# Performance work log

Hardware: AMD Instinct MI355X
Metric: run time of the kernel (lower is better)

Reference implementation:

```python
import jax, jax.numpy as jnp
import numpy as np

B, N, Hh, E = 16, 1024, 8, 64      # q/k/v: (B, N, H, E), H*E == ich
C, K, ICH, MODES = 64, 8, 512, 16  # c, k, ich, modes
IN_CH, OUT_CH, LVL = 64, 64, 0     # in_channels, out_channels, L


def fourier_cross_attn(q, k, v):
    """FourierCrossAttentionW with activation='tanh'. q,k,v: (B,L,E,H) -> (B,L,E,H).
    mode_select indices are range(min(L//2, modes)) -> contiguous low-mode slice.
    Note: v is unused in the original (only its length, equal to k's here)."""
    L = q.shape[1]
    xq = jnp.transpose(q, (0, 3, 2, 1))  # (B,H,E,L)
    xk = jnp.transpose(k, (0, 3, 2, 1))
    m = min(L // 2, MODES)
    xq_ft = jnp.fft.rfft(xq, axis=-1)[..., :m]   # (B,H,E,m) complex
    xk_ft = jnp.fft.rfft(xk, axis=-1)[..., :m]
    xqk = jnp.tanh(jnp.einsum('bhex,bhey->bhxy', xq_ft, xk_ft))  # complex tanh, (B,H,m,m)
    xqkv = jnp.einsum('bhxy,bhey->bhex', xqk, xk_ft)             # (B,H,E,m)
    pad = jnp.zeros(xqkv.shape[:-1] + (L // 2 + 1 - m,), xqkv.dtype)
    out_ft = jnp.concatenate([xqkv, pad], axis=-1)               # scatter low modes, rest zero
    out = jnp.fft.irfft(out_ft / (IN_CH * OUT_CH), n=L, axis=-1)
    return jnp.transpose(out, (0, 3, 2, 1))


def wavelet_transform(x, ec_d, ec_s):
    # x: (B, L, c, k) -> detail, approx each (B, L//2, c, k)
    xa = jnp.concatenate([x[:, ::2], x[:, 1::2]], axis=-1)  # (B, L/2, c, 2k)
    return xa @ ec_d, xa @ ec_s


def even_odd(x, rc_e, rc_o):
    # x: (B, L, c, 2k) -> (B, 2L, c, k), interleaving even/odd reconstructions
    b, n, c, _ = x.shape
    x_e = x @ rc_e  # (B,L,c,k)
    x_o = x @ rc_o
    return jnp.stack([x_e, x_o], axis=2).reshape(b, 2 * n, c, K)


def _forward(q, k, v, Lq_w, Lq_b, Lk_w, Lk_b, Lv_w, Lv_b, out_w, out_b,
             ec_s, ec_d, rc_e, rc_o):
    b, n, _, _ = q.shape
    s = k.shape[1]
    q = (q.reshape(b, n, ICH) @ Lq_w + Lq_b).reshape(b, n, C, K)
    k = (k.reshape(b, s, ICH) @ Lk_w + Lk_b).reshape(b, s, C, K)
    v = (v.reshape(b, s, ICH) @ Lv_w + Lv_b).reshape(b, s, C, K)
    if n > s:
        z = jnp.zeros((b, n - s, C, K), q.dtype)
        v = jnp.concatenate([v, z], axis=1)
        k = jnp.concatenate([k, z], axis=1)
    else:
        v = v[:, :n]
        k = k[:, :n]
    ns = int(np.floor(np.log2(n)))
    nl = 2 ** int(np.ceil(np.log2(n)))
    if nl > n:  # pad to power of two by wrapping leading entries
        q = jnp.concatenate([q, q[:, :nl - n]], axis=1)
        k = jnp.concatenate([k, k[:, :nl - n]], axis=1)
        v = jnp.concatenate([v, v[:, :nl - n]], axis=1)
    Ud, Us = [], []
    for _ in range(ns - LVL):
        dq, q = wavelet_transform(q, ec_d, ec_s)
        dk, k = wavelet_transform(k, ec_d, ec_s)
        dv, v = wavelet_transform(v, ec_d, ec_s)
        # original: attn1(d_q,d_k,d_v) + attn2(s_q,s_k,s_v); Us uses details (Us_q stores d)
        Ud.append(fourier_cross_attn(dq, dk, dv) + fourier_cross_attn(q, k, v))
        Us.append(fourier_cross_attn(dq, dk, dv))
    v = fourier_cross_attn(q, k, v)
    for i in range(ns - 1 - LVL, -1, -1):
        v = v + Us[i]
        v = jnp.concatenate([v, Ud[i]], axis=-1)
        v = even_odd(v, rc_e, rc_o)
    return v[:, :n].reshape(b, n, C * K) @ out_w + out_b


def setup_inputs() -> dict:
    key = jax.random.key(0)
    ks = jax.random.split(key, 16)
    f = jax.random.normal
    ws = 1.0 / np.sqrt(ICH)       # Linear init scale
    fs = 1.0 / np.sqrt(2 * K)     # wavelet filter scale (stand-in for legendre filters)
    return {
        'q': f(ks[0], (B, N, Hh, E), jnp.float32),
        'k': f(ks[1], (B, N, Hh, E), jnp.float32),
        'v': f(ks[2], (B, N, Hh, E), jnp.float32),
        'Lq_w': f(ks[3], (ICH, C * K), jnp.float32) * ws,
        'Lq_b': f(ks[4], (C * K,), jnp.float32) * ws,
        'Lk_w': f(ks[5], (ICH, C * K), jnp.float32) * ws,
        'Lk_b': f(ks[6], (C * K,), jnp.float32) * ws,
        'Lv_w': f(ks[7], (ICH, C * K), jnp.float32) * ws,
        'Lv_b': f(ks[8], (C * K,), jnp.float32) * ws,
        'out_w': f(ks[9], (C * K, ICH), jnp.float32) * ws,
        'out_b': f(ks[10], (ICH,), jnp.float32) * ws,
        'ec_s': f(ks[11], (2 * K, K), jnp.float32) * fs,
        'ec_d': f(ks[12], (2 * K, K), jnp.float32) * fs,
        'rc_e': f(ks[13], (2 * K, K), jnp.float32) * fs,
        'rc_o': f(ks[14], (2 * K, K), jnp.float32) * fs,
    }


def reference(q, k, v, Lq_w, Lq_b, Lk_w, Lk_b, Lv_w, Lv_b, out_w, out_b,
              ec_s, ec_d, rc_e, rc_o):
    return _forward(q, k, v, Lq_w, Lq_b, Lk_w, Lk_b, Lv_w, Lv_b,
                    out_w, out_b, ec_s, ec_d, rc_e, rc_o)
```

## Files before the change

kernel.cpp:

```cpp
#include <hip/hip_runtime.h>
#include <cstddef>

#define PI2F 6.283185307179586f

typedef __bf16 bf16_t;
typedef __bf16 bf16x8 __attribute__((ext_vector_type(8)));
typedef float f32x4 __attribute__((ext_vector_type(4)));

#define QA_OFF   0u
#define KA_OFF   8388608u
#define CH_OFF   16777216u
#define MF_OFF   (CH_OFF + 33488896u)
#define MUS_OFF  (MF_OFF + 9437184u)
#define MUD_OFF  (MUS_OFF + 2359296u)
#define WF_OFF   (MUD_OFF + 2359296u)
#define WI_OFF   (WF_OFF + 32704u)
#define WT_OFF   (WI_OFF + 32704u)

__global__ __launch_bounds__(256)
void wprep_k(const float* __restrict__ Wq, const float* __restrict__ Wk,
             const float* __restrict__ Wo, bf16_t* __restrict__ WT)
{
    __shared__ float T[32][33];
    const int w = blockIdx.x >> 8;
    const int tile = blockIdx.x & 255;
    const int k0 = (tile & 15) * 32, n0 = (tile >> 4) * 32;
    const float* W = (w == 0) ? Wq : (w == 1) ? Wk : Wo;
    bf16_t* oh = WT + (size_t)w * 524288;
    bf16_t* ol = oh + 262144;
    const int tid = threadIdx.x;
    {
        int row = tid >> 3, q = tid & 7;
        float4 v = *(const float4*)(W + (size_t)(k0 + row) * 512 + n0 + q * 4);
        T[row][q*4+0] = v.x; T[row][q*4+1] = v.y; T[row][q*4+2] = v.z; T[row][q*4+3] = v.w;
    }
    __syncthreads();
    {
        int nr = tid >> 3, q = tid & 7;
        union { bf16_t b[4]; uint2 u; } ph, pl;
#pragma unroll
        for (int j = 0; j < 4; ++j) {
            float x = T[q*4+j][nr];
            bf16_t h = (bf16_t)x;
            ph.b[j] = h;
            pl.b[j] = (bf16_t)(x - (float)h);
        }
        size_t dst = (size_t)(n0 + nr) * 512 + k0 + q * 4;
        *(uint2*)&oh[dst] = ph.u;
        *(uint2*)&ol[dst] = pl.u;
    }
}

template<bool TOUT>
__global__ __launch_bounds__(256)
void mfma_gemm_k(const float* __restrict__ X, const bf16_t* __restrict__ WTh,
                 const bf16_t* __restrict__ WTl, const float* __restrict__ bias,
                 float* __restrict__ out)
{
    __shared__ __align__(16) char smem[40960];
    bf16_t* Ah = (bf16_t*)smem;
    bf16_t* Al = Ah + 128 * 40;
    bf16_t* Bh = Al + 128 * 40;
    bf16_t* Bl = Bh + 128 * 40;
    float* Cs = (float*)smem;
    const int tid = threadIdx.x;
    const int lane = tid & 63;
    const int wv = tid >> 6;
    const int wm = wv & 1, wn = wv >> 1;
    const int m0 = blockIdx.x << 7, n0 = blockIdx.y << 7;
    const int l15 = lane & 15, quad = lane >> 4;

    f32x4 acc[4][4];
    f32x4 zz = {0.f, 0.f, 0.f, 0.f};
#pragma unroll
    for (int i = 0; i < 4; ++i)
#pragma unroll
        for (int j = 0; j < 4; ++j) acc[i][j] = zz;

    for (int kc = 0; kc < 16; ++kc) {
#pragma unroll
        for (int i = 0; i < 4; ++i) {
            int u = tid + i * 256;
            int row = u >> 3, seg = u & 7;
            float4 v = *(const float4*)(X + (size_t)(m0 + row) * 512 + kc * 32 + seg * 4);
            union { bf16_t b[4]; uint2 u2; } ph, pl;
            float xs[4] = {v.x, v.y, v.z, v.w};
#pragma unroll
            for (int j = 0; j < 4; ++j) {
                bf16_t h = (bf16_t)xs[j];
                ph.b[j] = h;
                pl.b[j] = (bf16_t)(xs[j] - (float)h);
            }
            *(uint2*)&Ah[row * 40 + seg * 4] = ph.u2;
            *(uint2*)&Al[row * 40 + seg * 4] = pl.u2;
        }
#pragma unroll
        for (int i = 0; i < 4; ++i) {
            int u = tid + i * 256;
            int variant = u >> 9;
            int rs = u & 511;
            int row = rs >> 2, seg = rs & 3;
            const bf16_t* src = (variant ? WTl : WTh) + (size_t)(n0 + row) * 512 + kc * 32 + seg * 8;
            bf16_t* dst = (variant ? Bl : Bh) + row * 40 + seg * 8;
            *(float4*)dst = *(const float4*)src;
        }
        __syncthreads();
        bf16x8 ah[4], al[4];
#pragma unroll
        for (int mi = 0; mi < 4; ++mi) {
            int row = wm * 64 + mi * 16 + l15;
            ah[mi] = *(bf16x8*)&Ah[row * 40 + quad * 8];
            al[mi] = *(bf16x8*)&Al[row * 40 + quad * 8];
        }
#pragma unroll
        for (int ni = 0; ni < 4; ++ni) {
            int nr = wn * 64 + ni * 16 + l15;
            bf16x8 bh = *(bf16x8*)&Bh[nr * 40 + quad * 8];
            bf16x8 bl = *(bf16x8*)&Bl[nr * 40 + quad * 8];
#pragma unroll
            for (int mi = 0; mi < 4; ++mi) {
                acc[mi][ni] = __builtin_amdgcn_mfma_f32_16x16x32_bf16(ah[mi], bh, acc[mi][ni], 0, 0, 0);
                acc[mi][ni] = __builtin_amdgcn_mfma_f32_16x16x32_bf16(ah[mi], bl, acc[mi][ni], 0, 0, 0);
                acc[mi][ni] = __builtin_amdgcn_mfma_f32_16x16x32_bf16(al[mi], bh, acc[mi][ni], 0, 0, 0);
            }
        }
        __syncthreads();
    }

    if constexpr (TOUT) {
        const int b8 = (m0 >> 10) * 8, tb = m0 & 1023;
        for (int p = 0; p < 2; ++p) {
            if (wn == p) {
#pragma unroll
                for (int ni = 0; ni < 4; ++ni)
#pragma unroll
                    for (int mi = 0; mi < 4; ++mi)
#pragma unroll
                        for (int r = 0; r < 4; ++r) {
                            int nl = ni * 16 + l15;
                            int m = wm * 64 + mi * 16 + quad * 4 + r;
                            Cs[nl * 132 + m] = acc[mi][ni][r];
                        }
            }
            __syncthreads();
#pragma unroll
            for (int i = 0; i < 8; ++i) {
                int u = tid + i * 256;
                int col = u >> 5, seg = u & 31;
                int gc = n0 + p * 64 + col;
                float bz = bias[gc];
                float4 v = *(float4*)&Cs[col * 132 + seg * 4];
                v.x += bz; v.y += bz; v.z += bz; v.w += bz;
                int h = gc & 7, e = gc >> 3;
                *(float4*)(out + (((size_t)(b8 + h)) * 64 + e) * 1024 + tb + seg * 4) = v;
            }
            __syncthreads();
        }
    } else {
#pragma unroll
        for (int ni = 0; ni < 4; ++ni) {
            int n = n0 + wn * 64 + ni * 16 + l15;
            float bz = bias[n];
#pragma unroll
            for (int mi = 0; mi < 4; ++mi)
#pragma unroll
                for (int r = 0; r < 4; ++r) {
                    int m = m0 + wm * 64 + mi * 16 + quad * 4 + r;
                    out[(size_t)m * 512 + n] = acc[mi][ni][r] + bz;
                }
        }
    }
}

__global__ __launch_bounds__(256)
void twiddle_k(float* __restrict__ Wf, float* __restrict__ Wi)
{
    int idx = blockIdx.x * 256 + threadIdx.x;
    int table = idx / 32704;
    if (table >= 2) return;
    int r = idx - table * 32704;
    int lvl = 0, base = 0;
    for (int l = 0; l < 9; ++l) {
        int Ll = 512 >> l;
        int sz = 32 * Ll;
        if (r < base + sz) { lvl = l; break; }
        base += sz;
    }
    int L = 512 >> lvl;
    int rr = r - base;
    if (table == 0) {
        int t = rr >> 5, c = rr & 31;
        int j = c & 15, isIm = c >> 4;
        int mv = (j * t) & (L - 1);
        float ang = (PI2F / (float)L) * (float)mv;
        float s, cc; sincosf(ang, &s, &cc);
        Wf[r] = isIm ? -s : cc;
    } else {
        int k = rr / L, t = rr - (rr / L) * L;
        int j = k & 15, isIm = k >> 4;
        int mv = (j * t) & (L - 1);
        float ang = (PI2F / (float)L) * (float)mv;
        float s, cc; sincosf(ang, &s, &cc);
        float scale = 1.f / (4096.f * (float)L);
        float v;
        if (!isIm) v = (j == 0) ? 1.f : 2.f * cc;
        else       v = (j == 0) ? 0.f : -2.f * s;
        Wi[r] = v * scale;
    }
}

__global__ __launch_bounds__(256)
void wavelet_chain_k(const float* __restrict__ qin, const float* __restrict__ kin,
                     float* __restrict__ CH,
                     const float* __restrict__ ecd, const float* __restrict__ ecs)
{
    __shared__ float sA[8][520];
    __shared__ float sB[8][264];
    __shared__ float fd[128], fs[128];
    const int tid = threadIdx.x;
    const int tensor = blockIdx.x >> 10;
    const int b = (blockIdx.x >> 6) & 15;
    const int e = blockIdx.x & 63;
    const float* in = tensor ? kin : qin;
    if (tid < 128) fd[tid] = ecd[tid];
    else fs[tid - 128] = ecs[tid - 128];
    __syncthreads();

    const size_t rowd0 = (size_t)((tensor * 2 + 0) * 8192) + (size_t)(b * 8) * 64 + e;

    {
        const int L = 512;
#pragma unroll
        for (int it = 0; it < 2; ++it) {
            const int t = tid + it * 256;
            float xa[16];
#pragma unroll
            for (int h = 0; h < 8; ++h) {
                float2 v = *(const float2*)(in + ((size_t)((b*8 + h) * 64 + e)) * 1024 + 2 * t);
                xa[h] = v.x; xa[8 + h] = v.y;
            }
#pragma unroll
            for (int jj = 0; jj < 8; ++jj) {
                float ad = 0.f, as_ = 0.f;
#pragma unroll
                for (int rr = 0; rr < 16; ++rr) {
                    ad  = fmaf(xa[rr], fd[rr * 8 + jj], ad);
                    as_ = fmaf(xa[rr], fs[rr * 8 + jj], as_);
                }
                size_t rowd = rowd0 + (size_t)jj * 64;
                CH[rowd * L + t]          = ad;
                CH[(rowd + 8192) * L + t] = as_;
                sA[jj][t] = as_;
            }
        }
    }
    __syncthreads();

    float* cur = &sA[0][0]; int cs = 520;
    float* nxt = &sB[0][0]; int ns = 264;
    for (int lvl = 1; lvl < 9; ++lvl) {
        const int L = 512 >> lvl;
        const size_t chb = (size_t)32768 * (size_t)(1024 - 2 * L);
        if (tid < L) {
            const int t = tid;
            float xa[16];
#pragma unroll
            for (int h = 0; h < 8; ++h) {
                xa[h]     = cur[h * cs + 2 * t];
                xa[8 + h] = cur[h * cs + 2 * t + 1];
            }
#pragma unroll
            for (int jj = 0; jj < 8; ++jj) {
                float ad = 0.f, as_ = 0.f;
#pragma unroll
                for (int rr = 0; rr < 16; ++rr) {
                    ad  = fmaf(xa[rr], fd[rr * 8 + jj], ad);
                    as_ = fmaf(xa[rr], fs[rr * 8 + jj], as_);
                }
                size_t rowd = rowd0 + (size_t)jj * 64;
                CH[chb + rowd * L + t]          = ad;
                CH[chb + (rowd + 8192) * L + t] = as_;
                nxt[jj * ns + t] = as_;
            }
        }
        __syncthreads();
        float* tp = cur; cur = nxt; nxt = tp;
        int ts_ = cs; cs = ns; ns = ts_;
    }
}

__global__ __launch_bounds__(256)
void fwd_dft_k(const float* __restrict__ CH, const float* __restrict__ Wf,
               float* __restrict__ MF)
{
    __shared__ float As[32][132];
    __shared__ float Ws[32][36];
    const int tid = threadIdx.x;
    const int lvl = blockIdx.x >> 8;
    const int tile = blockIdx.x & 255;
    const int L = 512 >> lvl;
    const size_t chb = (size_t)32768 * (size_t)(1024 - 2 * L);
    const int wb = 32 * (1024 - 2 * L);
    const size_t mfb = (size_t)lvl * 1048576;
    const int rowb = tile * 128;
    const int rg = tid >> 3, cg = tid & 7;
    float acc[4][4] = {{0.f}};
    const int kw = (L < 32) ? L : 32;

    for (int k0 = 0; k0 < L; k0 += kw) {
        if (kw >= 4) {
            const int kq = kw >> 2;
            const int kqs = (kq == 8) ? 3 : (kq == 4) ? 2 : (kq == 2) ? 1 : 0;
            const int nf4 = 128 * kq;
            for (int u = tid; u < nf4; u += 256) {
                int row = u >> kqs, q = u & (kq - 1);
                float4 v = *(const float4*)(CH + chb + (size_t)(rowb + row) * L + k0 + q * 4);
                As[q*4+0][row] = v.x; As[q*4+1][row] = v.y;
                As[q*4+2][row] = v.z; As[q*4+3][row] = v.w;
            }
        } else {
            if (tid < 256) {
                int row = tid >> 1, t = tid & 1;
                As[t][row] = CH[chb + (size_t)(rowb + row) * 2 + t];
            }
        }
        for (int u = tid; u < kw * 8; u += 256) {
            int kr = u >> 3, q = u & 7;
            *(float4*)&Ws[kr][q * 4] = *(const float4*)&Wf[wb + (k0 + kr) * 32 + q * 4];
        }
        __syncthreads();
#pragma unroll 4
        for (int kk = 0; kk < kw; ++kk) {
            float4 a4 = *(float4*)&As[kk][rg * 4];
            float4 w4 = *(float4*)&Ws[kk][cg * 4];
            acc[0][0] = fmaf(a4.x, w4.x, acc[0][0]); acc[0][1] = fmaf(a4.x, w4.y, acc[0][1]);
            acc[0][2] = fmaf(a4.x, w4.z, acc[0][2]); acc[0][3] = fmaf(a4.x, w4.w, acc[0][3]);
            acc[1][0] = fmaf(a4.y, w4.x, acc[1][0]); acc[1][1] = fmaf(a4.y, w4.y, acc[1][1]);
            acc[1][2] = fmaf(a4.y, w4.z, acc[1][2]); acc[1][3] = fmaf(a4.y, w4.w, acc[1][3]);
            acc[2][0] = fmaf(a4.z, w4.x, acc[2][0]); acc[2][1] = fmaf(a4.z, w4.y, acc[2][1]);
            acc[2][2] = fmaf(a4.z, w4.z, acc[2][2]); acc[2][3] = fmaf(a4.z, w4.w, acc[2][3]);
            acc[3][0] = fmaf(a4.w, w4.x, acc[3][0]); acc[3][1] = fmaf(a4.w, w4.y, acc[3][1]);
            acc[3][2] = fmaf(a4.w, w4.z, acc[3][2]); acc[3][3] = fmaf(a4.w, w4.w, acc[3][3]);
        }
        __syncthreads();
    }
#pragma unroll
    for (int i = 0; i < 4; ++i) {
        float4 o = {acc[i][0], acc[i][1], acc[i][2], acc[i][3]};
        *(float4*)(MF + mfb + (size_t)(rowb + rg * 4 + i) * 32 + cg * 4) = o;
    }
}

__global__ __launch_bounds__(256)
void combine2_k(const float* __restrict__ MF, float* __restrict__ MUS, float* __restrict__ MUD)
{
    __shared__ float F[4][64][33];
    __shared__ float Sre[2][16][17], Sim[2][16][17];
    const int tid = threadIdx.x;
    const int lvl = blockIdx.x >> 7;
    const int bh = blockIdx.x & 127;
    const int L = 512 >> lvl;
    const int m = (L / 2 < 16) ? L / 2 : 16;
    const size_t mfb = (size_t)lvl * 1048576;
    for (int a = 0; a < 4; ++a) {
        const float* src = MF + mfb + ((size_t)a * 8192 + (size_t)bh * 64) * 32;
        for (int u = tid; u < 512; u += 256) {
            float4 v = *(const float4*)(src + u * 4);
            int ee = (u * 4) >> 5, c = (u * 4) & 31;
            F[a][ee][c] = v.x; F[a][ee][c+1] = v.y; F[a][ee][c+2] = v.z; F[a][ee][c+3] = v.w;
        }
    }
    __syncthreads();
    const int mm = m * m;
    for (int idx = tid; idx < 2 * mm; idx += 256) {
        int p = idx / mm, rr = idx - p * mm;
        int x = rr / m, y = rr - (rr / m) * m;
        float sr = 0.f, si = 0.f;
        for (int ee = 0; ee < 64; ++ee) {
            float qre = F[p][ee][x],     qim = F[p][ee][16 + x];
            float kre = F[2 + p][ee][y], kim = F[2 + p][ee][16 + y];
            sr = fmaf(qre, kre, sr); sr = fmaf(-qim, kim, sr);
            si = fmaf(qre, kim, si); si = fmaf(qim, kre, si);
        }
        float twoa = fminf(fmaxf(2.f * sr, -30.f), 30.f);
        float e2 = expf(twoa), inv = 1.f / e2;
        float s2b, c2b; sincosf(2.f * si, &s2b, &c2b);
        float den = 0.5f * (e2 + inv) + c2b;
        Sre[p][x][y] = 0.5f * (e2 - inv) / den;
        Sim[p][x][y] = s2b / den;
    }
    __syncthreads();
    for (int idx = tid; idx < 1024; idx += 256) {
        int ee = idx >> 4, x = idx & 15;
        float urd = 0.f, uid = 0.f, urs = 0.f, uis = 0.f;
        if (x < m) {
            for (int y = 0; y < m; ++y) {
                float k0re = F[2][ee][y], k0im = F[2][ee][16 + y];
                float k1re = F[3][ee][y], k1im = F[3][ee][16 + y];
                float s0r = Sre[0][x][y], s0i = Sim[0][x][y];
                float s1r = Sre[1][x][y], s1i = Sim[1][x][y];
                urd = fmaf(s0r, k0re, urd); urd = fmaf(-s0i, k0im, urd);
                uid = fmaf(s0r, k0im, uid); uid = fmaf(s0i, k0re, uid);
                urs = fmaf(s1r, k1re, urs); urs = fmaf(-s1i, k1im, urs);
                uis = fmaf(s1r, k1im, uis); uis = fmaf(s1i, k1re, uis);
            }
        }
        size_t mb = (size_t)lvl * 262144 + ((size_t)bh * 64 + ee) * 32;
        MUS[mb + x]      = urd;
        MUS[mb + 16 + x] = uid;
        MUD[mb + x]      = urd + urs;
        MUD[mb + 16 + x] = uid + uis;
    }
}

__global__ __launch_bounds__(256)
void inv_dft_k(const float* __restrict__ MUS, const float* __restrict__ MUD,
               const float* __restrict__ Wi,
               float* __restrict__ US, float* __restrict__ UD)
{
    __shared__ float As[32][132];
    __shared__ float Ws[32][36];
    const int bx = blockIdx.x;
    int lvl = 0, base = 0;
#pragma unroll
    for (int l = 0; l < 9; ++l) {
        int cl = 128 << ((l <= 4) ? (4 - l) : 0);
        if (bx < base + cl) { lvl = l; break; }
        base += cl;
    }
    const int r = bx - base;
    const int L = 512 >> lvl;
    const int tcb = (lvl <= 4) ? (4 - lvl) : 0;
    const int tile = r >> tcb;
    const int tc = r & ((1 << tcb) - 1);
    const int t0 = tc * 32;
    const int ar = tile >> 6;
    const int rowb = (tile & 63) * 128;
    const float* MU = ar ? MUD : MUS;
    float* OUT = ar ? UD : US;
    const int wb = 32 * (1024 - 2 * L);
    const size_t uoff = (size_t)8192 * (size_t)(1024 - 2 * L);
    const int nc = (L < 32) ? L : 32;
    const int tid = threadIdx.x;
    const int rg = tid >> 3, cg = tid & 7;

#pragma unroll
    for (int i = 0; i < 4; ++i) {
        int u = tid + i * 256;
        int row = u >> 3, q = u & 7;
        float4 v = *(const float4*)(MU + (size_t)lvl * 262144 + (size_t)(rowb + row) * 32 + q * 4);
        As[q*4+0][row] = v.x; As[q*4+1][row] = v.y;
        As[q*4+2][row] = v.z; As[q*4+3][row] = v.w;
    }
    if (L >= 4) {
        int ncq = nc >> 2;
        int bits = (nc == 32) ? 3 : (nc == 16) ? 2 : (nc == 8) ? 1 : 0;
        for (int u = tid; u < 32 * ncq; u += 256) {
            int kr = u >> bits, q = u & (ncq - 1);
            *(float4*)&Ws[kr][q * 4] = *(const float4*)&Wi[wb + kr * L + t0 + q * 4];
        }
    } else {
        for (int u = tid; u < 64; u += 256)
            Ws[u >> 1][u & 1] = Wi[wb + (u >> 1) * 2 + (u & 1)];
    }
    __syncthreads();
    if (cg * 4 < nc) {
        float acc[4][4] = {{0.f}};
#pragma unroll 8
        for (int kk = 0; kk < 32; ++kk) {
            float4 a4 = *(float4*)&As[kk][rg * 4];
            float4 w4 = *(float4*)&Ws[kk][cg * 4];
            acc[0][0] = fmaf(a4.x, w4.x, acc[0][0]); acc[0][1] = fmaf(a4.x, w4.y, acc[0][1]);
            acc[0][2] = fmaf(a4.x, w4.z, acc[0][2]); acc[0][3] = fmaf(a4.x, w4.w, acc[0][3]);
            acc[1][0] = fmaf(a4.y, w4.x, acc[1][0]); acc[1][1] = fmaf(a4.y, w4.y, acc[1][1]);
            acc[1][2] = fmaf(a4.y, w4.z, acc[1][2]); acc[1][3] = fmaf(a4.y, w4.w, acc[1][3]);
            acc[2][0] = fmaf(a4.z, w4.x, acc[2][0]); acc[2][1] = fmaf(a4.z, w4.y, acc[2][1]);
            acc[2][2] = fmaf(a4.z, w4.z, acc[2][2]); acc[2][3] = fmaf(a4.z, w4.w, acc[2][3]);
            acc[3][0] = fmaf(a4.w, w4.x, acc[3][0]); acc[3][1] = fmaf(a4.w, w4.y, acc[3][1]);
            acc[3][2] = fmaf(a4.w, w4.z, acc[3][2]); acc[3][3] = fmaf(a4.w, w4.w, acc[3][3]);
        }
        if (L >= 4) {
#pragma unroll
            for (int i = 0; i < 4; ++i) {
                float4 o = {acc[i][0], acc[i][1], acc[i][2], acc[i][3]};
                *(float4*)(OUT + uoff + (size_t)(rowb + rg * 4 + i) * L + t0 + cg * 4) = o;
            }
        } else {
#pragma unroll
            for (int i = 0; i < 4; ++i) {
                OUT[uoff + (size_t)(rowb + rg * 4 + i) * 2 + 0] = acc[i][0];
                OUT[uoff + (size_t)(rowb + rg * 4 + i) * 2 + 1] = acc[i][1];
            }
        }
    }
}

__global__ __launch_bounds__(256)
void recon_all_k(const float* __restrict__ USg, const float* __restrict__ UDg,
                 const float* __restrict__ rce, const float* __restrict__ rco,
                 float* __restrict__ vT)
{
    __shared__ float v[8][1032];
    __shared__ float se[16][8];
    __shared__ float so[16][8];
    const int tid = threadIdx.x;
    const int b = blockIdx.x >> 6;
    const int e = blockIdx.x & 63;
    if (tid < 128) se[tid >> 3][tid & 7] = rce[tid];
    else { int u = tid - 128; so[u >> 3][u & 7] = rco[u]; }
    if (tid < 16) v[tid >> 1][tid & 1] = 0.f;
    __syncthreads();

    for (int i = 8; i >= 0; --i) {
        const int L = 512 >> i;
        const size_t uoff = (size_t)8192 * (1024 - 2 * L);
        const int nC = (L + 255) >> 8;
        for (int c = nC - 1; c >= 0; --c) {
            const int t = (c << 8) + tid;
            float a[16];
            const bool act = t < L;
            if (act) {
#pragma unroll
                for (int h = 0; h < 8; ++h) {
                    size_t pgl = uoff + ((size_t)((b*8 + h) * 64 + e)) * (size_t)L + t;
                    a[h]     = v[h][t] + USg[pgl];
                    a[8 + h] = UDg[pgl];
                }
            }
            __syncthreads();
            if (act) {
#pragma unroll
                for (int jj = 0; jj < 8; ++jj) {
                    float ev = 0.f, od = 0.f;
#pragma unroll
                    for (int rr = 0; rr < 16; ++rr) {
                        ev = fmaf(a[rr], se[rr][jj], ev);
                        od = fmaf(a[rr], so[rr][jj], od);
                    }
                    v[jj][2 * t]     = ev;
                    v[jj][2 * t + 1] = od;
                }
            }
            __syncthreads();
        }
    }
    for (int u = tid; u < 2048; u += 256) {
        int h = u >> 8, q4 = u & 255;
        float4 val = *(float4*)&v[h][q4 * 4];
        *(float4*)(vT + ((size_t)((b*8 + h) * 64 + e)) * 1024 + q4 * 4) = val;
    }
}

__global__ __launch_bounds__(256)
void trans_tn_k(const float* __restrict__ vT, float* __restrict__ vN)
{
    __shared__ float Ls[512][17];
    const int b = blockIdx.x >> 6;
    const int t0 = (blockIdx.x & 63) << 4;
    const int tid = threadIdx.x;
#pragma unroll
    for (int it = 0; it < 8; ++it) {
        int u = it * 256 + tid;
        int row = u >> 2, part = u & 3;
        float4 v = *(const float4*)(vT + ((size_t)b * 512 + row) * 1024 + t0 + part * 4);
        Ls[row][part*4+0] = v.x;
        Ls[row][part*4+1] = v.y;
        Ls[row][part*4+2] = v.z;
        Ls[row][part*4+3] = v.w;
    }
    __syncthreads();
#pragma unroll
    for (int it = 0; it < 8; ++it) {
        int u = it * 256 + tid;
        int cq = u & 127, tt = u >> 7;
        int c = cq * 4;
        float4 v;
        v.x = Ls[(((c+0) & 7) << 6) + ((c+0) >> 3)][tt];
        v.y = Ls[(((c+1) & 7) << 6) + ((c+1) >> 3)][tt];
        v.z = Ls[(((c+2) & 7) << 6) + ((c+2) >> 3)][tt];
        v.w = Ls[(((c+3) & 7) << 6) + ((c+3) >> 3)][tt];
        *(float4*)(vN + ((size_t)b * 1024 + t0 + tt) * 512 + c) = v;
    }
}

extern "C" void kernel_launch(void* const* d_in, const int* in_sizes, int n_in,
                              void* d_out, int out_size, void* d_ws, size_t ws_size,
                              hipStream_t stream)
{
    const float* q    = (const float*)d_in[0];
    const float* k    = (const float*)d_in[1];
    const float* Lq_w = (const float*)d_in[3];
    const float* Lq_b = (const float*)d_in[4];
    const float* Lk_w = (const float*)d_in[5];
    const float* Lk_b = (const float*)d_in[6];
    const float* outw = (const float*)d_in[9];
    const float* outb = (const float*)d_in[10];
    const float* ec_s = (const float*)d_in[11];
    const float* ec_d = (const float*)d_in[12];
    const float* rc_e = (const float*)d_in[13];
    const float* rc_o = (const float*)d_in[14];

    float* ws = (float*)d_ws;
    float* qA  = ws + QA_OFF;
    float* kA  = ws + KA_OFF;
    float* CH  = ws + CH_OFF;
    float* MF  = ws + MF_OFF;
    float* MUS = ws + MUS_OFF;
    float* MUD = ws + MUD_OFF;
    float* Wf  = ws + WF_OFF;
    float* Wi  = ws + WI_OFF;
    bf16_t* WT = (bf16_t*)(ws + WT_OFF);
    float* vT  = CH;
    float* vN  = CH + 8388608;

    twiddle_k<<<256, 256, 0, stream>>>(Wf, Wi);
    wprep_k<<<768, 256, 0, stream>>>(Lq_w, Lk_w, outw, WT);

    dim3 gg(128, 4);
    mfma_gemm_k<true><<<gg, 256, 0, stream>>>(q, WT, WT + 262144, Lq_b, qA);
    mfma_gemm_k<true><<<gg, 256, 0, stream>>>(k, WT + 524288, WT + 786432, Lk_b, kA);

    wavelet_chain_k<<<2048, 256, 0, stream>>>(qA, kA, CH, ec_d, ec_s);
    fwd_dft_k<<<2304, 256, 0, stream>>>(CH, Wf, MF);
    combine2_k<<<1152, 256, 0, stream>>>(MF, MUS, MUD);
    inv_dft_k<<<4480, 256, 0, stream>>>(MUS, MUD, Wi, qA, kA);
    recon_all_k<<<1024, 256, 0, stream>>>(qA, kA, rc_e, rc_o, vT);
    trans_tn_k<<<1024, 256, 0, stream>>>(vT, vN);
    mfma_gemm_k<false><<<gg, 256, 0, stream>>>(vN, WT + 1048576, WT + 1310720, outb, (float*)d_out);
}
```

Measured before the change: 575.1 us.

## Split wavelet decomposition chain into per-level parallel kernels

Replaces the single wavelet_chain_k, where one block per column ran all nine levels with shrinking thread utilization, with separate launches. Levels 0-3 each get a wide grid that tiles the sequence, reading the previous level's approximation back from global CH. A final kernel handles levels 4-8 in shared memory. This gives much more parallelism and better occupancy for the early levels, at the cost of extra launches and re-reading intermediate approximations from global memory.

```diff
diff --git a/kernel.cpp b/kernel.cpp
--- a/kernel.cpp
+++ b/kernel.cpp
@@ -210,78 +210,94 @@
 }
 
 __global__ __launch_bounds__(256)
-void wavelet_chain_k(const float* __restrict__ qin, const float* __restrict__ kin,
-                     float* __restrict__ CH,
-                     const float* __restrict__ ecd, const float* __restrict__ ecs)
-{
-    __shared__ float sA[8][520];
-    __shared__ float sB[8][264];
+void wavelet_lvl_k(const float* __restrict__ in_t0, const float* __restrict__ in_t1,
+                   float* __restrict__ CH,
+                   const float* __restrict__ ecd, const float* __restrict__ ecs,
+                   int L, int inLen, int nt)
+{
+    __shared__ float sIn[8][132];
+    __shared__ float fd[128], fs[128];
+    const int tid = threadIdx.x;
+    const int col = blockIdx.x / nt;
+    const int tc = blockIdx.x - col * nt;
+    const int tensor = col >> 10;
+    const int b = (col >> 6) & 15;
+    const int e = col & 63;
+    if (tid < 128) fd[tid] = ecd[tid];
+    else fs[tid - 128] = ecs[tid - 128];
+    const float* in = tensor ? in_t1 : in_t0;
+    {
+        int h = tid >> 5, q = tid & 31;
+        *(float4*)&sIn[h][q * 4] =
+            *(const float4*)(in + (size_t)((b*8 + h) * 64 + e) * (size_t)inLen + tc * 128 + q * 4);
+    }
+    __syncthreads();
+    const int jj2 = tid >> 6, t = tid & 63;
+    float xa[16];
+#pragma unroll
+    for (int h = 0; h < 8; ++h) {
+        xa[h]     = sIn[h][2 * t];
+        xa[8 + h] = sIn[h][2 * t + 1];
+    }
+    const size_t rowd0 = (size_t)(tensor * 2) * 8192 + (size_t)(b * 8) * 64 + e;
+    const size_t chb = (size_t)32768 * (size_t)(1024 - 2 * L);
+    const int tg = tc * 64 + t;
+#pragma unroll
+    for (int jq = 0; jq < 2; ++jq) {
+        int jj = jj2 * 2 + jq;
+        float d = 0.f, s = 0.f;
+#pragma unroll
+        for (int rr = 0; rr < 16; ++rr) {
+            d = fmaf(xa[rr], fd[rr * 8 + jj], d);
+            s = fmaf(xa[rr], fs[rr * 8 + jj], s);
+        }
+        size_t rowd = rowd0 + (size_t)jj * 64;
+        CH[chb + rowd * (size_t)L + tg]          = d;
+        CH[chb + (rowd + 8192) * (size_t)L + tg] = s;
+    }
+}
+
+__global__ __launch_bounds__(256)
+void wavelet_deep_k(const float* __restrict__ in_t0, const float* __restrict__ in_t1,
+                    float* __restrict__ CH,
+                    const float* __restrict__ ecd, const float* __restrict__ ecs)
+{
+    __shared__ float sP[8][66];
+    __shared__ float sN[8][34];
     __shared__ float fd[128], fs[128];
     const int tid = threadIdx.x;
     const int tensor = blockIdx.x >> 10;
     const int b = (blockIdx.x >> 6) & 15;
     const int e = blockIdx.x & 63;
-    const float* in = tensor ? kin : qin;
     if (tid < 128) fd[tid] = ecd[tid];
     else fs[tid - 128] = ecs[tid - 128];
-    __syncthreads();
-
-    const size_t rowd0 = (size_t)((tensor * 2 + 0) * 8192) + (size_t)(b * 8) * 64 + e;
-
-    {
-        const int L = 512;
-#pragma unroll
-        for (int it = 0; it < 2; ++it) {
-            const int t = tid + it * 256;
-            float xa[16];
-#pragma unroll
-            for (int h = 0; h < 8; ++h) {
-                float2 v = *(const float2*)(in + ((size_t)((b*8 + h) * 64 + e)) * 1024 + 2 * t);
-                xa[h] = v.x; xa[8 + h] = v.y;
-            }
-#pragma unroll
-            for (int jj = 0; jj < 8; ++jj) {
-                float ad = 0.f, as_ = 0.f;
-#pragma unroll
-                for (int rr = 0; rr < 16; ++rr) {
-                    ad  = fmaf(xa[rr], fd[rr * 8 + jj], ad);
-                    as_ = fmaf(xa[rr], fs[rr * 8 + jj], as_);
-                }
-                size_t rowd = rowd0 + (size_t)jj * 64;
-                CH[rowd * L + t]          = ad;
-                CH[(rowd + 8192) * L + t] = as_;
-                sA[jj][t] = as_;
-            }
-        }
-    }
-    __syncthreads();
-
-    float* cur = &sA[0][0]; int cs = 520;
-    float* nxt = &sB[0][0]; int ns = 264;
-    for (int lvl = 1; lvl < 9; ++lvl) {
+    const float* in = tensor ? in_t1 : in_t0;
+    if (tid < 128) {
+        int h = tid >> 4, q = tid & 15;
+        *(float4*)&sP[h][q * 4] =
+            *(const float4*)(in + (size_t)((b*8 + h) * 64 + e) * 64 + q * 4);
+    }
+    __syncthreads();
+    float* cur = &sP[0][0]; int cs = 66;
+    float* nxt = &sN[0][0]; int ns = 34;
+    const size_t rowd0 = (size_t)(tensor * 2) * 8192 + (size_t)(b * 8) * 64 + e;
+    for (int lvl = 4; lvl < 9; ++lvl) {
         const int L = 512 >> lvl;
         const size_t chb = (size_t)32768 * (size_t)(1024 - 2 * L);
-        if (tid < L) {
-            const int t = tid;
-            float xa[16];
-#pragma unroll
-            for (int h = 0; h < 8; ++h) {
-                xa[h]     = cur[h * cs + 2 * t];
-                xa[8 + h] = cur[h * cs + 2 * t + 1];
-            }
-#pragma unroll
-            for (int jj = 0; jj < 8; ++jj) {
-                float ad = 0.f, as_ = 0.f;
-#pragma unroll
-                for (int rr = 0; rr < 16; ++rr) {
-                    ad  = fmaf(xa[rr], fd[rr * 8 + jj], ad);
-                    as_ = fmaf(xa[rr], fs[rr * 8 + jj], as_);
-                }
-                size_t rowd = rowd0 + (size_t)jj * 64;
-                CH[chb + rowd * L + t]          = ad;
-                CH[chb + (rowd + 8192) * L + t] = as_;
-                nxt[jj * ns + t] = as_;
-            }
+        if (tid < 8 * L) {
+            const int jj = tid / L;
+            const int t = tid - jj * L;
+            float d = 0.f, s = 0.f;
+#pragma unroll
+            for (int rr = 0; rr < 16; ++rr) {
+                float x = (rr < 8) ? cur[rr * cs + 2 * t] : cur[(rr - 8) * cs + 2 * t + 1];
+                d = fmaf(x, fd[rr * 8 + jj], d);
+                s = fmaf(x, fs[rr * 8 + jj], s);
+            }
+            size_t rowd = rowd0 + (size_t)jj * 64;
+            CH[chb + rowd * (size_t)L + t]          = d;
+            CH[chb + (rowd + 8192) * (size_t)L + t] = s;
+            nxt[jj * ns + t] = s;
         }
         __syncthreads();
         float* tp = cur; cur = nxt; nxt = tp;
@@ -620,7 +636,23 @@
     mfma_gemm_k<true><<<gg, 256, 0, stream>>>(q, WT, WT + 262144, Lq_b, qA);
     mfma_gemm_k<true><<<gg, 256, 0, stream>>>(k, WT + 524288, WT + 786432, Lk_b, kA);
 
-    wavelet_chain_k<<<2048, 256, 0, stream>>>(qA, kA, CH, ec_d, ec_s);
+    wavelet_lvl_k<<<16384, 256, 0, stream>>>(qA, kA, CH, ec_d, ec_s, 512, 1024, 8);
+    for (int lvl = 1; lvl <= 3; ++lvl) {
+        int L = 512 >> lvl;
+        int Lp = 2 * L;
+        size_t chbp = (size_t)32768 * (size_t)(1024 - 2 * Lp);
+        const float* i0 = CH + chbp + (size_t)8192 * Lp;
+        const float* i1 = CH + chbp + (size_t)24576 * Lp;
+        int nt = L / 64;
+        wavelet_lvl_k<<<2048 * nt, 256, 0, stream>>>(i0, i1, CH, ec_d, ec_s, L, Lp, nt);
+    }
+    {
+        size_t chbp = (size_t)32768 * (size_t)(1024 - 128);
+        const float* i0 = CH + chbp + (size_t)8192 * 64;
+        const float* i1 = CH + chbp + (size_t)24576 * 64;
+        wavelet_deep_k<<<2048, 256, 0, stream>>>(i0, i1, CH, ec_d, ec_s);
+    }
+
     fwd_dft_k<<<2304, 256, 0, stream>>>(CH, Wf, MF);
     combine2_k<<<1152, 256, 0, stream>>>(MF, MUS, MUD);
     inv_dft_k<<<4480, 256, 0, stream>>>(MUS, MUD, Wi, qA, kA);
```

Result: faster. 486.1 us (-15.5%).
